# Kernel optimization log

Measured on AMD Instinct MI355X. Metric: run time of the kernel, lower is better.

Reference implementation:

```python
import jax, jax.numpy as jnp
import numpy as np

B, IN, H = 4096, 2048, 2048
STD = 1.0 / np.sqrt(H)


def setup_inputs() -> dict:
    key = jax.random.key(0)
    ks = jax.random.split(key, 16)
    uni = lambda k, shape: jax.random.uniform(k, shape, jnp.float32, -STD, STD)
    inp = {
        "x": jax.random.normal(ks[0], (B, IN), jnp.float32),
        "h": jax.random.normal(ks[1], (B, H), jnp.float32),
        "c": jax.random.normal(ks[2], (B, H), jnp.float32),
        # weights are used untransposed via th.mm(x, w): w_x* must be [IN, H]-compatible,
        # which in the original requires IN == H; shapes kept as [H, IN].
        "w_xi": uni(ks[3], (H, IN)), "w_xf": uni(ks[4], (H, IN)),
        "w_xo": uni(ks[5], (H, IN)), "w_xc": uni(ks[6], (H, IN)),
        "w_hi": uni(ks[7], (H, H)), "w_hf": uni(ks[8], (H, H)),
        "w_ho": uni(ks[9], (H, H)), "w_hc": uni(ks[10], (H, H)),
        "b_i": uni(ks[11], (H,)), "b_f": uni(ks[12], (H,)),
        "b_o": uni(ks[13], (H,)), "b_c": uni(ks[14], (H,)),
    }
    return inp


def reference(x, h, c, w_xi, w_xf, w_xo, w_xc, w_hi, w_hf, w_ho, w_hc,
              b_i, b_f, b_o, b_c):
    # Fused form of the 8 small GEMMs: concat gate weights along output dim.
    Wx = jnp.concatenate([w_xi, w_xf, w_xo, w_xc], axis=1)  # [IN, 4H]
    Wh = jnp.concatenate([w_hi, w_hf, w_ho, w_hc], axis=1)  # [H, 4H]
    b = jnp.concatenate([b_i, b_f, b_o, b_c])               # [4H]
    gates = x @ Wx + h @ Wh + b                              # [B, 4H]
    i_t, f_t, o_t, g_t = jnp.split(gates, 4, axis=1)
    i_t = jax.nn.sigmoid(i_t)
    f_t = jax.nn.sigmoid(f_t)
    o_t = jax.nn.sigmoid(o_t)
    g_t = jnp.tanh(g_t)
    c_t = c * f_t + i_t * g_t
    h_t = o_t * jnp.tanh(c_t)
    # original reshapes to [B, 1, H]
    return h_t[:, None, :], c_t[:, None, :]
```

## Files before the change

### kernel.cpp

```cpp
#include <hip/hip_runtime.h>
#include <stdint.h>

typedef unsigned short u16;
typedef __bf16 bf16x8 __attribute__((ext_vector_type(8)));
typedef float f32x4 __attribute__((ext_vector_type(4)));
typedef unsigned short u16x8 __attribute__((ext_vector_type(8)));
typedef unsigned short u16x4 __attribute__((ext_vector_type(4)));

#define B_ROWS 4096
#define H_DIM  2048
#define K_DIM  4096
#define N_DIM  8192

__device__ __forceinline__ u16 f2b(float f) {
  union { float f; unsigned int i; } v; v.f = f;
  unsigned int i = v.i;
  return (u16)((i + 0x7fffu + ((i >> 16) & 1u)) >> 16);
}
__device__ __forceinline__ float b2f(u16 u) {
  union { unsigned int i; float f; } v; v.i = ((unsigned int)u) << 16; return v.f;
}
__device__ __forceinline__ float sigmoidf_(float x) { return 1.0f / (1.0f + __expf(-x)); }
__device__ __forceinline__ float tanhf_(float x)    { return 1.0f - 2.0f / (__expf(2.0f * x) + 1.0f); }

__device__ __forceinline__ void glds16(const u16* g, u16* l) {
  __builtin_amdgcn_global_load_lds(
      (__attribute__((address_space(1))) void*)(g),
      (__attribute__((address_space(3))) void*)(l), 16, 0, 0);
}

struct WPtrs { const float* p[8]; };

__global__ __launch_bounds__(256) void prep_all(WPtrs wp,
                                                const float* __restrict__ X,
                                                const float* __restrict__ Hs,
                                                u16* __restrict__ Wt,
                                                u16* __restrict__ Abf) {
  __shared__ float tile[64][65];
  const int z = blockIdx.z;
  const int tid = threadIdx.x;
  if (z < 8) {
    const int s = z >> 2, g = z & 3;
    const float* __restrict__ w = wp.p[z];
    const int j0 = blockIdx.x * 64, k0 = blockIdx.y * 64;

    const int c4 = (tid & 15) * 4;
    const int r0 = tid >> 4;
#pragma unroll
    for (int it = 0; it < 4; ++it) {
      int r = r0 + it * 16;
      float4 v = *(const float4*)(w + (size_t)(k0 + r) * H_DIM + j0 + c4);
      tile[r][c4 + 0] = v.x;
      tile[r][c4 + 1] = v.y;
      tile[r][c4 + 2] = v.z;
      tile[r][c4 + 3] = v.w;
    }
    __syncthreads();

    const int cc = (tid & 7) * 8;
    const int jr0 = tid >> 3;
#pragma unroll
    for (int it = 0; it < 2; ++it) {
      int jr = jr0 + it * 32;
      u16x8 v;
#pragma unroll
      for (int i = 0; i < 8; ++i) v[i] = f2b(tile[cc + i][jr]);
      size_t orow = (size_t)(g * H_DIM + j0 + jr);
      *(u16x8*)(Wt + orow * K_DIM + (size_t)(s * H_DIM + k0 + cc)) = v;
    }
  } else {
    const int cid = (z - 8) * 1024 + blockIdx.y * 32 + blockIdx.x;
#pragma unroll
    for (int t = 0; t < 4; ++t) {
      const size_t chunk = (size_t)cid * 1024 + t * 256 + tid;
      const int b = (int)(chunk >> 9);
      const int c = ((int)chunk & 511) * 8;
      const float* src = (c < H_DIM) ? (X + (size_t)b * H_DIM + c)
                                     : (Hs + (size_t)b * H_DIM + (c - H_DIM));
      float4 v0 = *(const float4*)(src);
      float4 v1 = *(const float4*)(src + 4);
      u16x8 o;
      o[0] = f2b(v0.x); o[1] = f2b(v0.y); o[2] = f2b(v0.z); o[3] = f2b(v0.w);
      o[4] = f2b(v1.x); o[5] = f2b(v1.y); o[6] = f2b(v1.z); o[7] = f2b(v1.w);
      *(u16x8*)(Abf + chunk * 8) = o;
    }
  }
}

__global__ __launch_bounds__(256) void gemm_gates(const u16* __restrict__ A,
                                                  const u16* __restrict__ Wt,
                                                  u16* __restrict__ gates) {
  __shared__ __align__(16) u16 sA[128 * 32];
  __shared__ __align__(16) u16 sB[128 * 32];
  const int tid = threadIdx.x;
  const int wave = tid >> 6, lane = tid & 63;
  const int bm = blockIdx.x & 31;
  const int bn = blockIdx.x >> 5;
  const int wr = (wave >> 1) * 64;
  const int wc = (wave & 1) * 64;

  const int c0 = wave * 2;
  const int row0 = c0 * 16 + (lane >> 2);
  const int row1 = row0 + 16;
  const int kc0 = (lane & 3) ^ ((row0 >> 1) & 3);
  const int kc1 = (lane & 3) ^ ((row1 >> 1) & 3);
  const size_t gA0 = (size_t)(bm * 128 + row0) * K_DIM + kc0 * 8;
  const size_t gA1 = (size_t)(bm * 128 + row1) * K_DIM + kc1 * 8;
  const size_t gB0 = (size_t)(bn * 128 + row0) * K_DIM + kc0 * 8;
  const size_t gB1 = (size_t)(bn * 128 + row1) * K_DIM + kc1 * 8;
  u16* ldsA0 = sA + c0 * 512;
  u16* ldsA1 = sA + (c0 + 1) * 512;
  u16* ldsB0 = sB + c0 * 512;
  u16* ldsB1 = sB + (c0 + 1) * 512;

  const int q = lane >> 4;
  int aOff[4], bOff[4];
#pragma unroll
  for (int i = 0; i < 4; ++i) {
    int ra = wr + i * 16 + (lane & 15);
    aOff[i] = ra * 32 + ((q ^ ((ra >> 1) & 3)) * 8);
    int rb = wc + i * 16 + (lane & 15);
    bOff[i] = rb * 32 + ((q ^ ((rb >> 1) & 3)) * 8);
  }

  f32x4 acc[4][4] = {};

  for (int kt = 0; kt < K_DIM / 32; ++kt) {
    const int kg = kt * 32;
    __syncthreads();
    glds16(A + gA0 + kg, ldsA0);
    glds16(A + gA1 + kg, ldsA1);
    glds16(Wt + gB0 + kg, ldsB0);
    glds16(Wt + gB1 + kg, ldsB1);
    __syncthreads();

    bf16x8 af[4], bf[4];
#pragma unroll
    for (int i = 0; i < 4; ++i) af[i] = *reinterpret_cast<const bf16x8*>(sA + aOff[i]);
#pragma unroll
    for (int i = 0; i < 4; ++i) bf[i] = *reinterpret_cast<const bf16x8*>(sB + bOff[i]);
#pragma unroll
    for (int mi = 0; mi < 4; ++mi)
#pragma unroll
      for (int ni = 0; ni < 4; ++ni)
        acc[mi][ni] = __builtin_amdgcn_mfma_f32_16x16x32_bf16(af[mi], bf[ni], acc[mi][ni], 0, 0, 0);
  }

  const int rbase = bm * 128 + wr + (lane >> 4) * 4;
  const int cbase = bn * 128 + wc + (lane & 15);
#pragma unroll
  for (int mi = 0; mi < 4; ++mi) {
#pragma unroll
    for (int ni = 0; ni < 4; ++ni) {
      size_t base = (size_t)(rbase + mi * 16) * N_DIM + (size_t)(cbase + ni * 16);
#pragma unroll
      for (int r = 0; r < 4; ++r)
        gates[base + (size_t)r * N_DIM] = f2b(acc[mi][ni][r]);
    }
  }
}

__global__ __launch_bounds__(256) void lstm_epilogue(
    const u16* __restrict__ gates, const float* __restrict__ Cin,
    const float* __restrict__ Bi, const float* __restrict__ Bf,
    const float* __restrict__ Bo, const float* __restrict__ Bc,
    float* __restrict__ Out) {
  const int idx = blockIdx.x * 256 + threadIdx.x;
  const int b = idx >> 9;
  const int j = (idx & 511) * 4;
  const size_t gbase = (size_t)b * N_DIM + j;
  u16x4 iv = *(const u16x4*)(gates + gbase);
  u16x4 fv = *(const u16x4*)(gates + gbase + 2048);
  u16x4 ov = *(const u16x4*)(gates + gbase + 4096);
  u16x4 gv = *(const u16x4*)(gates + gbase + 6144);
  float4 cv  = *(const float4*)(Cin + (size_t)b * H_DIM + j);
  float4 biv = *(const float4*)(Bi + j);
  float4 bfv = *(const float4*)(Bf + j);
  float4 bov = *(const float4*)(Bo + j);
  float4 bcv = *(const float4*)(Bc + j);
  float ce[4] = {cv.x, cv.y, cv.z, cv.w};
  float bie[4] = {biv.x, biv.y, biv.z, biv.w};
  float bfe[4] = {bfv.x, bfv.y, bfv.z, bfv.w};
  float boe[4] = {bov.x, bov.y, bov.z, bov.w};
  float bce[4] = {bcv.x, bcv.y, bcv.z, bcv.w};
  float4 hv, ctv;
  float he[4], cte[4];
#pragma unroll
  for (int e = 0; e < 4; ++e) {
    float it = sigmoidf_(b2f(iv[e]) + bie[e]);
    float ft = sigmoidf_(b2f(fv[e]) + bfe[e]);
    float ot = sigmoidf_(b2f(ov[e]) + boe[e]);
    float gt = tanhf_(b2f(gv[e]) + bce[e]);
    float ct = ce[e] * ft + it * gt;
    he[e] = ot * tanhf_(ct);
    cte[e] = ct;
  }
  hv.x = he[0]; hv.y = he[1]; hv.z = he[2]; hv.w = he[3];
  ctv.x = cte[0]; ctv.y = cte[1]; ctv.z = cte[2]; ctv.w = cte[3];
  *(float4*)(Out + (size_t)b * H_DIM + j) = hv;
  *(float4*)(Out + (size_t)B_ROWS * H_DIM + (size_t)b * H_DIM + j) = ctv;
}

extern "C" void kernel_launch(void* const* d_in, const int* in_sizes, int n_in,
                              void* d_out, int out_size, void* d_ws, size_t ws_size,
                              hipStream_t stream) {
  const float* X   = (const float*)d_in[0];
  const float* Hs  = (const float*)d_in[1];
  const float* Cin = (const float*)d_in[2];
  WPtrs wp;
  for (int i = 0; i < 8; ++i) wp.p[i] = (const float*)d_in[3 + i];
  const float* Bi = (const float*)d_in[11];
  const float* Bf = (const float*)d_in[12];
  const float* Bo = (const float*)d_in[13];
  const float* Bc = (const float*)d_in[14];

  u16* Wt    = (u16*)d_ws;
  u16* Abf   = Wt + (size_t)N_DIM * K_DIM;
  u16* gates = Abf + (size_t)B_ROWS * K_DIM;
  float* Out = (float*)d_out;

  prep_all<<<dim3(32, 32, 10), 256, 0, stream>>>(wp, X, Hs, Wt, Abf);
  gemm_gates<<<32 * 64, 256, 0, stream>>>(Abf, Wt, gates);
  lstm_epilogue<<<(B_ROWS * H_DIM / 4) / 256, 256, 0, stream>>>(gates, Cin, Bi, Bf, Bo, Bc, Out);
}
```

Before: 570.8 us.

## Rewrite GEMM as 256x256 tiles with 4-stage LDS pipeline and XCD-aware block mapping

The gates GEMM moves from 128x128 tiles with 4 waves and a synchronous load-compute loop to 256x256 tiles with 8 waves, each wave computing a 128x64 subtile. Direct global-to-LDS loads run through a 4-buffer ring with 3 tiles prefetched. Explicit vmcnt waits and raw barriers replace __syncthreads, and s_setprio raises priority around the MFMA bursts. The block index is remapped so consecutive blocks sharing tiles land on the same XCD, which should improve L2 reuse. The goal is to hide global load latency and raise arithmetic intensity, at the cost of 128 KB of LDS, more accumulator registers and tricky synchronisation.

```diff
diff --git a/kernel.cpp b/kernel.cpp
--- a/kernel.cpp
+++ b/kernel.cpp
@@ -87,69 +87,111 @@
   }
 }
 
-__global__ __launch_bounds__(256) void gemm_gates(const u16* __restrict__ A,
-                                                  const u16* __restrict__ Wt,
-                                                  u16* __restrict__ gates) {
-  __shared__ __align__(16) u16 sA[128 * 32];
-  __shared__ __align__(16) u16 sB[128 * 32];
+__global__ __launch_bounds__(512, 2) void gemm_gates(const u16* __restrict__ A,
+                                                     const u16* __restrict__ Wt,
+                                                     u16* __restrict__ gates) {
+  __shared__ __align__(16) u16 sA[4 * 256 * 32];
+  __shared__ __align__(16) u16 sB[4 * 256 * 32];
   const int tid = threadIdx.x;
   const int wave = tid >> 6, lane = tid & 63;
-  const int bm = blockIdx.x & 31;
-  const int bn = blockIdx.x >> 5;
-  const int wr = (wave >> 1) * 64;
-  const int wc = (wave & 1) * 64;
+  const int wm = wave >> 2, wn = wave & 3;
+
+  const int wg = (blockIdx.x & 7) * 64 + (blockIdx.x >> 3);
+  const int bm = wg & 15;
+  const int bn = wg >> 4;
 
   const int c0 = wave * 2;
-  const int row0 = c0 * 16 + (lane >> 2);
-  const int row1 = row0 + 16;
-  const int kc0 = (lane & 3) ^ ((row0 >> 1) & 3);
-  const int kc1 = (lane & 3) ^ ((row1 >> 1) & 3);
-  const size_t gA0 = (size_t)(bm * 128 + row0) * K_DIM + kc0 * 8;
-  const size_t gA1 = (size_t)(bm * 128 + row1) * K_DIM + kc1 * 8;
-  const size_t gB0 = (size_t)(bn * 128 + row0) * K_DIM + kc0 * 8;
-  const size_t gB1 = (size_t)(bn * 128 + row1) * K_DIM + kc1 * 8;
-  u16* ldsA0 = sA + c0 * 512;
-  u16* ldsA1 = sA + (c0 + 1) * 512;
-  u16* ldsB0 = sB + c0 * 512;
-  u16* ldsB1 = sB + (c0 + 1) * 512;
+  const int rs0 = c0 * 16 + (lane >> 2);
+  const int rs1 = rs0 + 16;
+  const int kc0 = (lane & 3) ^ ((rs0 >> 1) & 3);
+  const int kc1 = (lane & 3) ^ ((rs1 >> 1) & 3);
+  const size_t gA0 = (size_t)(bm * 256 + rs0) * K_DIM + kc0 * 8;
+  const size_t gA1 = (size_t)(bm * 256 + rs1) * K_DIM + kc1 * 8;
+  const size_t gB0 = (size_t)(bn * 256 + rs0) * K_DIM + kc0 * 8;
+  const size_t gB1 = (size_t)(bn * 256 + rs1) * K_DIM + kc1 * 8;
 
   const int q = lane >> 4;
-  int aOff[4], bOff[4];
+  int aOff[8], bOff[4];
+#pragma unroll
+  for (int i = 0; i < 8; ++i) {
+    int ra = wm * 128 + i * 16 + (lane & 15);
+    aOff[i] = ra * 32 + ((q ^ ((ra >> 1) & 3)) * 8);
+  }
 #pragma unroll
   for (int i = 0; i < 4; ++i) {
-    int ra = wr + i * 16 + (lane & 15);
-    aOff[i] = ra * 32 + ((q ^ ((ra >> 1) & 3)) * 8);
-    int rb = wc + i * 16 + (lane & 15);
+    int rb = wn * 64 + i * 16 + (lane & 15);
     bOff[i] = rb * 32 + ((q ^ ((rb >> 1) & 3)) * 8);
   }
 
-  f32x4 acc[4][4] = {};
-
-  for (int kt = 0; kt < K_DIM / 32; ++kt) {
-    const int kg = kt * 32;
-    __syncthreads();
-    glds16(A + gA0 + kg, ldsA0);
-    glds16(A + gA1 + kg, ldsA1);
-    glds16(Wt + gB0 + kg, ldsB0);
-    glds16(Wt + gB1 + kg, ldsB1);
-    __syncthreads();
-
+  f32x4 acc[8][4] = {};
+  const int NT = K_DIM / 32;
+
+#pragma unroll
+  for (int t = 0; t < 3; ++t) {
+    const size_t ko = (size_t)t * 32;
+    u16* da = sA + t * 8192;
+    u16* db = sB + t * 8192;
+    glds16(A  + gA0 + ko, da + c0 * 512);
+    glds16(A  + gA1 + ko, da + (c0 + 1) * 512);
+    glds16(Wt + gB0 + ko, db + c0 * 512);
+    glds16(Wt + gB1 + ko, db + (c0 + 1) * 512);
+  }
+  asm volatile("s_waitcnt vmcnt(8)" ::: "memory");
+  __builtin_amdgcn_s_barrier();
+
+  for (int T = 0; T < NT; ++T) {
+    u16* sAs = sA + (T & 3) * 8192;
+    u16* sBs = sB + (T & 3) * 8192;
+    const int pf = T + 3;
+    const bool dopf = pf < NT;
+    const size_t ko = (size_t)pf * 32;
+    u16* dA = sA + (pf & 3) * 8192;
+    u16* dB = sB + (pf & 3) * 8192;
+
+    if (dopf) {
+      glds16(A + gA0 + ko, dA + c0 * 512);
+      glds16(A + gA1 + ko, dA + (c0 + 1) * 512);
+    }
     bf16x8 af[4], bf[4];
 #pragma unroll
-    for (int i = 0; i < 4; ++i) af[i] = *reinterpret_cast<const bf16x8*>(sA + aOff[i]);
-#pragma unroll
-    for (int i = 0; i < 4; ++i) bf[i] = *reinterpret_cast<const bf16x8*>(sB + bOff[i]);
+    for (int i = 0; i < 4; ++i) af[i] = *reinterpret_cast<const bf16x8*>(sAs + aOff[i]);
+#pragma unroll
+    for (int i = 0; i < 4; ++i) bf[i] = *reinterpret_cast<const bf16x8*>(sBs + bOff[i]);
+    __builtin_amdgcn_s_barrier();
+    __builtin_amdgcn_s_setprio(1);
 #pragma unroll
     for (int mi = 0; mi < 4; ++mi)
 #pragma unroll
       for (int ni = 0; ni < 4; ++ni)
         acc[mi][ni] = __builtin_amdgcn_mfma_f32_16x16x32_bf16(af[mi], bf[ni], acc[mi][ni], 0, 0, 0);
-  }
-
-  const int rbase = bm * 128 + wr + (lane >> 4) * 4;
-  const int cbase = bn * 128 + wc + (lane & 15);
-#pragma unroll
-  for (int mi = 0; mi < 4; ++mi) {
+    __builtin_amdgcn_s_setprio(0);
+
+    if (dopf) {
+      glds16(Wt + gB0 + ko, dB + c0 * 512);
+      glds16(Wt + gB1 + ko, dB + (c0 + 1) * 512);
+    }
+    bf16x8 ag[4];
+#pragma unroll
+    for (int i = 0; i < 4; ++i) ag[i] = *reinterpret_cast<const bf16x8*>(sAs + aOff[4 + i]);
+    __builtin_amdgcn_s_barrier();
+    __builtin_amdgcn_s_setprio(1);
+#pragma unroll
+    for (int mi = 0; mi < 4; ++mi)
+#pragma unroll
+      for (int ni = 0; ni < 4; ++ni)
+        acc[4 + mi][ni] = __builtin_amdgcn_mfma_f32_16x16x32_bf16(ag[mi], bf[ni], acc[4 + mi][ni], 0, 0, 0);
+    __builtin_amdgcn_s_setprio(0);
+
+    if (T < NT - 3)       { asm volatile("s_waitcnt vmcnt(8)" ::: "memory"); }
+    else if (T == NT - 3) { asm volatile("s_waitcnt vmcnt(4)" ::: "memory"); }
+    else if (T == NT - 2) { asm volatile("s_waitcnt vmcnt(0)" ::: "memory"); }
+    if (T < NT - 1) __builtin_amdgcn_s_barrier();
+  }
+
+  const int rbase = bm * 256 + wm * 128 + (lane >> 4) * 4;
+  const int cbase = bn * 256 + wn * 64 + (lane & 15);
+#pragma unroll
+  for (int mi = 0; mi < 8; ++mi) {
 #pragma unroll
     for (int ni = 0; ni < 4; ++ni) {
       size_t base = (size_t)(rbase + mi * 16) * N_DIM + (size_t)(cbase + ni * 16);
@@ -220,6 +262,6 @@
   float* Out = (float*)d_out;
 
   prep_all<<<dim3(32, 32, 10), 256, 0, stream>>>(wp, X, Hs, Wt, Abf);
-  gemm_gates<<<32 * 64, 256, 0, stream>>>(Abf, Wt, gates);
+  gemm_gates<<<16 * 32, 512, 0, stream>>>(Abf, Wt, gates);
   lstm_epilogue<<<(B_ROWS * H_DIM / 4) / 256, 256, 0, stream>>>(gates, Cin, Bi, Bf, Bo, Bc, Out);
 }
```

Result: no change. 580.2 us (+1.7%).
